# Kernel tuning notes

Measured on AMD Instinct MI355X. Metric: run time of the kernel, lower is better.

## Reference

```python
import jax, jax.numpy as jnp
import numpy as np

D = 64
N_NODES = 100000
N_EDGES = 1600000
N_GRAPHS = 64
IN_CH = 128
EDGE_DIM = 7
N_CONVS = 3  # layers after conv_first


def seg_softmax(logits, seg, n):
    m = jax.ops.segment_max(logits, seg, num_segments=n)
    e = jnp.exp(logits - m[seg])
    s = jax.ops.segment_sum(e, seg, num_segments=n)
    return e / (s[seg] + 1e-16)


def tconv(h, src, dst, edge_attr, Wq, bq, Wk, bk, Wv, bv, We, Ws, bs):
    # PyG TransformerConv, heads=1, concat=True, root_weight=True
    q = h @ Wq + bq          # [N, D]
    k = h @ Wk + bk
    v = h @ Wv + bv
    e = edge_attr @ We       # [E, D] (lin_edge has no bias)
    ke = k[src] + e          # key + edge per message
    alpha = jnp.sum(q[dst] * ke, axis=-1) / jnp.sqrt(jnp.float32(D))
    a = seg_softmax(alpha, dst, N_NODES)               # softmax over in-neighbors
    msg = a[:, None] * (v[src] + e)                    # [E, D]
    out = jax.ops.segment_sum(msg, dst, num_segments=N_NODES)
    return out + h @ Ws + bs                           # skip (lin_skip)


def setup_inputs() -> dict:
    key = jax.random.key(0)
    ks = iter(jax.random.split(key, 64))
    nrm = lambda shp, s=0.05: jax.random.normal(next(ks), shp, dtype=jnp.float32) * s
    inp = {}
    inp['x'] = jax.random.normal(next(ks), (N_NODES, IN_CH), dtype=jnp.float32)
    inp['edge_index'] = jax.random.randint(next(ks), (2, N_EDGES), 0, N_NODES, dtype=jnp.int32)
    inp['edge_attr'] = jax.random.normal(next(ks), (N_EDGES, EDGE_DIM), dtype=jnp.float32)
    inp['batch'] = jnp.sort(jax.random.randint(next(ks), (N_NODES,), 0, N_GRAPHS, dtype=jnp.int32))
    inp['y'] = jax.random.normal(next(ks), (N_GRAPHS, 6), dtype=jnp.float32)
    # conv_first (IN_CH -> D)
    inp['Wq0'] = nrm((IN_CH, D)); inp['bq0'] = jnp.zeros((D,), jnp.float32)
    inp['Wk0'] = nrm((IN_CH, D)); inp['bk0'] = jnp.zeros((D,), jnp.float32)
    inp['Wv0'] = nrm((IN_CH, D)); inp['bv0'] = jnp.zeros((D,), jnp.float32)
    inp['We0'] = nrm((EDGE_DIM, D))
    inp['Ws0'] = nrm((IN_CH, D)); inp['bs0'] = jnp.zeros((D,), jnp.float32)
    # stacked conv layers (D -> D), leading axis = layer
    inp['Wq'] = nrm((N_CONVS, D, D)); inp['bq'] = jnp.zeros((N_CONVS, D), jnp.float32)
    inp['Wk'] = nrm((N_CONVS, D, D)); inp['bk'] = jnp.zeros((N_CONVS, D), jnp.float32)
    inp['Wv'] = nrm((N_CONVS, D, D)); inp['bv'] = jnp.zeros((N_CONVS, D), jnp.float32)
    inp['We'] = nrm((N_CONVS, EDGE_DIM, D))
    inp['Ws'] = nrm((N_CONVS, D, D)); inp['bs'] = jnp.zeros((N_CONVS, D), jnp.float32)
    # gate_nn: Linear(D,D)+ReLU+Linear(D,1)
    inp['g1W'] = nrm((D, D)); inp['g1b'] = jnp.zeros((D,), jnp.float32)
    inp['g2W'] = nrm((D, 1)); inp['g2b'] = jnp.zeros((1,), jnp.float32)
    # 6 MLPs, each 64->32->16->8->1, stacked on leading expert axis
    inp['m0W'] = nrm((6, D, 32)); inp['m0b'] = jnp.zeros((6, 32), jnp.float32)
    inp['m1W'] = nrm((6, 32, 16)); inp['m1b'] = jnp.zeros((6, 16), jnp.float32)
    inp['m2W'] = nrm((6, 16, 8)); inp['m2b'] = jnp.zeros((6, 8), jnp.float32)
    inp['m3W'] = nrm((6, 8, 1)); inp['m3b'] = jnp.zeros((6, 1), jnp.float32)
    return inp


def reference(x, edge_attr, y, Wq0, bq0, Wk0, bk0, Wv0, bv0, We0, Ws0, bs0,
              Wq, bq, Wk, bk, Wv, bv, We, Ws, bs,
              g1W, g1b, g2W, g2b,
              m0W, m0b, m1W, m1b, m2W, m2b, m3W, m3b,
              edge_index, batch):
    src, dst = edge_index[0], edge_index[1]
    elu = jax.nn.elu
    outs = []
    h = elu(tconv(x, src, dst, edge_attr, Wq0, bq0, Wk0, bk0, Wv0, bv0, We0, Ws0, bs0))
    outs.append(h)
    for i in range(N_CONVS):
        h = tconv(h, src, dst, edge_attr, Wq[i], bq[i], Wk[i], bk[i],
                  Wv[i], bv[i], We[i], Ws[i], bs[i])
        if i != N_CONVS - 1:
            h = elu(h)
        outs.append(h)
    # JumpingKnowledge 'max'
    h = jnp.max(jnp.stack(outs, axis=0), axis=0)          # [N, D]
    # Global soft attention pooling
    gate = jax.nn.relu(h @ g1W + g1b) @ g2W + g2b         # [N, 1]
    gate = seg_softmax(gate[:, 0], batch, N_GRAPHS)[:, None]
    pooled = jax.ops.segment_sum(gate * h, batch, num_segments=N_GRAPHS)  # [G, D]
    # 6-way MLP ensemble (elu hidden)
    a = elu(jnp.einsum('gd,edh->egh', pooled, m0W) + m0b[:, None, :])
    a = elu(jnp.einsum('egh,ehk->egk', a, m1W) + m1b[:, None, :])
    a = elu(jnp.einsum('egk,ekj->egj', a, m2W) + m2b[:, None, :])
    preds = jnp.einsum('egj,ejo->ego', a, m3W) + m3b[:, None, :]  # [6, G, 1]
    preds = preds[:, :, 0].T                               # [G, 6]
    losses = jnp.sqrt(jnp.mean((preds - y) ** 2, axis=0))  # RMSE per target
    total_loss = jnp.sum(losses)
    return preds, total_loss
```

## Files before the change

### kernel.cpp

```cpp
#include <hip/hip_runtime.h>
#include <math.h>

#define N_NODES 100000
#define N_EDGES 1600000
#define N_GRAPHS 64
#define IN_CH 128
#define DIM 64
#define N_CONVS 3
#define NBLK 196
#define NPASS 8
#define PASS_SZ 12500

typedef const float* fp;
typedef unsigned int u32;
typedef unsigned short u16;
typedef __attribute__((ext_vector_type(8))) short short8v;
typedef __attribute__((ext_vector_type(4))) float f32x4;

__device__ inline u16 rne_bf16(float f) {
    u32 u = __float_as_uint(f);
    return (u16)((u + 0x7fffu + ((u >> 16) & 1u)) >> 16);
}
__device__ inline float bf16_f(u16 w) { return __uint_as_float((u32)w << 16); }
__device__ inline float bf16lo_f(u32 w) { return __uint_as_float(w << 16); }
__device__ inline float bf16hi_f(u32 w) { return __uint_as_float(w & 0xffff0000u); }
__device__ inline u32 f_enc(float f) {
    u32 u = __float_as_uint(f);
    return (u & 0x80000000u) ? ~u : (u | 0x80000000u);
}
__device__ inline float f_dec(u32 e) {
    u32 u = (e & 0x80000000u) ? (e & 0x7fffffffu) : ~e;
    return __uint_as_float(u);
}

__global__ __launch_bounds__(256) void count_kernel(const int* __restrict__ dst, int* __restrict__ cnt) {
    int j = blockIdx.x * 256 + threadIdx.x;
    if (j < N_EDGES) {
        int d = dst[j];
        if ((unsigned)d < N_NODES) atomicAdd(&cnt[d], 1);
    }
}

__global__ __launch_bounds__(512) void scan1_kernel(const int* __restrict__ cnt, int* __restrict__ rp,
                                                    int* __restrict__ blksum) {
    __shared__ int tmp[512];
    int t = threadIdx.x, i = blockIdx.x * 512 + t;
    int v0 = (i < N_NODES) ? cnt[i] : 0;
    tmp[t] = v0;
    __syncthreads();
    for (int off = 1; off < 512; off <<= 1) {
        int add = (t >= off) ? tmp[t - off] : 0;
        __syncthreads();
        tmp[t] += add;
        __syncthreads();
    }
    if (i < N_NODES) rp[i] = tmp[t] - v0;
    if (t == 511) blksum[blockIdx.x] = tmp[511];
}

__global__ __launch_bounds__(256) void scan2_kernel(int* __restrict__ blksum) {
    __shared__ int tmp[256];
    int t = threadIdx.x;
    int v0 = (t < NBLK) ? blksum[t] : 0;
    tmp[t] = v0;
    __syncthreads();
    for (int off = 1; off < 256; off <<= 1) {
        int add = (t >= off) ? tmp[t - off] : 0;
        __syncthreads();
        tmp[t] += add;
        __syncthreads();
    }
    if (t < NBLK) blksum[t] = tmp[t] - v0;
}

__global__ __launch_bounds__(512) void scan3_kernel(int* __restrict__ rp, const int* __restrict__ blksum,
                                                    int* __restrict__ cursor) {
    int t = threadIdx.x, i = blockIdx.x * 512 + t;
    if (i < N_NODES) {
        int v = rp[i] + blksum[blockIdx.x];
        rp[i] = v;
        cursor[i] = v;
    }
    if (i == 0) rp[N_NODES] = N_EDGES;
}

__global__ __launch_bounds__(256) void scatter_pass_kernel(const int* __restrict__ src,
                                                           const int* __restrict__ dst, fp ea,
                                                           int* __restrict__ cursor,
                                                           int* __restrict__ csr_src,
                                                           uint4* __restrict__ eab, int lo, int hi) {
    int j = blockIdx.x * 256 + threadIdx.x;
    if (j < N_EDGES) {
        int d = dst[j];
        if (d < lo || d >= hi || (unsigned)d >= N_NODES) return;
        int pos = atomicAdd(&cursor[d], 1);
        if ((unsigned)pos < N_EDGES) {
            int s = src[j];
            csr_src[pos] = ((unsigned)s < N_NODES) ? s : 0;
            size_t sb = (size_t)j * 7;
            u16 b[8];
#pragma unroll
            for (int c = 0; c < 7; ++c) b[c] = rne_bf16(ea[sb + c]);
            b[7] = 0;
            uint4 o;
            o.x = b[0] | ((u32)b[1] << 16);
            o.y = b[2] | ((u32)b[3] << 16);
            o.z = b[4] | ((u32)b[5] << 16);
            o.w = b[6] | ((u32)b[7] << 16);
            eab[pos] = o;
        }
    }
}

__global__ __launch_bounds__(256) void cvt_bf16_kernel(const float* __restrict__ in, u16* __restrict__ out,
                                                       int n4) {
    int i = blockIdx.x * 256 + threadIdx.x;
    if (i < n4) {
        float4 v = reinterpret_cast<const float4*>(in)[i];
        ushort4 o;
        o.x = rne_bf16(v.x); o.y = rne_bf16(v.y); o.z = rne_bf16(v.z); o.w = rne_bf16(v.w);
        reinterpret_cast<ushort4*>(out)[i] = o;
    }
}

__global__ __launch_bounds__(256) void packW_kernel(fp Wq, fp Wk, fp Wv, fp Ws, u16* __restrict__ Bp,
                                                    int K) {
    int total = (K / 32) * 16 * 512;
    int tid = blockIdx.x * 256 + threadIdx.x;
    if (tid >= total) return;
    int j = tid & 7, l = (tid >> 3) & 63, fragid = tid >> 9;
    int tk = fragid >> 4, gtn = fragid & 15;
    int k = tk * 32 + ((l >> 4) << 3) + j;
    int n = (gtn << 4) + (l & 15);
    int mat = n >> 6, cn = n & 63;
    fp W = mat == 0 ? Wq : mat == 1 ? Wk : mat == 2 ? Wv : Ws;
    Bp[tid] = rne_bf16(W[k * 64 + cn]);
}

template <int K>
__global__ __launch_bounds__(256) void gemm_mfma_kernel(
    const u16* __restrict__ A, const u16* __restrict__ Bp,
    fp bq, fp bk, fp bv, fp bs,
    u16* __restrict__ qb, u32* __restrict__ kvp, u16* __restrict__ skbb) {
    constexpr int NTK = K / 32;
    __shared__ u16 kls[32][64];
    int wave = threadIdx.x >> 6;
    int l = threadIdx.x & 63;
    int lr = l & 15, lg = l >> 4;
    int row0 = blockIdx.x * 32;
    short8v a[2][NTK];
#pragma unroll
    for (int mi = 0; mi < 2; ++mi)
#pragma unroll
        for (int tk = 0; tk < NTK; ++tk)
            a[mi][tk] = *reinterpret_cast<const short8v*>(
                &A[(size_t)(row0 + mi * 16 + lr) * K + tk * 32 + lg * 8]);
    f32x4 c[2][4] = {};
#pragma unroll
    for (int tn = 0; tn < 4; ++tn) {
        int gtn = wave * 4 + tn;
#pragma unroll
        for (int tk = 0; tk < NTK; ++tk) {
            short8v b = *reinterpret_cast<const short8v*>(&Bp[((size_t)(tk * 16 + gtn) * 64 + l) * 8]);
            c[0][tn] = __builtin_amdgcn_mfma_f32_16x16x32_bf16(a[0][tk], b, c[0][tn], 0, 0, 0);
            c[1][tn] = __builtin_amdgcn_mfma_f32_16x16x32_bf16(a[1][tk], b, c[1][tn], 0, 0, 0);
        }
    }
    fp bias = wave == 0 ? bq : wave == 1 ? bk : wave == 2 ? bv : bs;
    if (wave == 1) {
#pragma unroll
        for (int tn = 0; tn < 4; ++tn) {
            int cl = tn * 16 + lr;
            float bb = bias[cl];
#pragma unroll
            for (int mi = 0; mi < 2; ++mi)
#pragma unroll
                for (int r = 0; r < 4; ++r) {
                    int rr = mi * 16 + lg * 4 + r;
                    kls[rr][cl] = rne_bf16(c[mi][tn][r] + bb);
                }
        }
    }
    __syncthreads();
    if (wave == 1) return;
#pragma unroll
    for (int tn = 0; tn < 4; ++tn) {
        int cl = tn * 16 + lr;
        float bb = bias[cl];
#pragma unroll
        for (int mi = 0; mi < 2; ++mi)
#pragma unroll
            for (int r = 0; r < 4; ++r) {
                int rr = mi * 16 + lg * 4 + r;
                size_t row = row0 + rr;
                float val = c[mi][tn][r] + bb;
                if (wave == 0) qb[row * 64 + cl] = rne_bf16(val * 0.125f);
                else if (wave == 3) skbb[row * 64 + cl] = rne_bf16(val);
                else kvp[row * 64 + cl] = (u32)kls[rr][cl] | ((u32)rne_bf16(val) << 16);
            }
    }
}

__global__ __launch_bounds__(256) void node_kernel(
    const u16* __restrict__ qb, const u32* __restrict__ kvp,
    const u16* __restrict__ skbb, const uint4* __restrict__ eab, fp We,
    const int* __restrict__ row_ptr, const int* __restrict__ csr_src,
    u16* __restrict__ hb, u16* __restrict__ hmaxb, int act, int initmax) {
    int tid = threadIdx.x;
    int lane = tid & 63;
    int g = lane >> 4, fl = lane & 15;
    int n = blockIdx.x * 4 + (tid >> 6);
    int f0 = fl * 4;
    ushort4 qv = *reinterpret_cast<const ushort4*>(&qb[(size_t)n * 64 + f0]);
    float4 q4;
    q4.x = bf16_f(qv.x); q4.y = bf16_f(qv.y); q4.z = bf16_f(qv.z); q4.w = bf16_f(qv.w);
    float qw_own = 0.f;
#pragma unroll
    for (int c = 0; c < 7; ++c) {
        float4 w4 = *reinterpret_cast<const float4*>(&We[c * 64 + f0]);
        float t = q4.x * w4.x + q4.y * w4.y + q4.z * w4.z + q4.w * w4.w;
        t += __shfl_xor(t, 1);
        t += __shfl_xor(t, 2);
        t += __shfl_xor(t, 4);
        t += __shfl_xor(t, 8);
        if (fl == c) qw_own = t;
    }
    int beg = row_ptr[n], end = row_ptr[n + 1];
    float s = 0.f;
    float ax = 0.f, ay = 0.f, az = 0.f, aw = 0.f;
    float r_own = 0.f;

    for (int p0 = beg; p0 < end; p0 += 64) {
        int navail = end - p0;
        if (navail > 64) navail = 64;
        int sv = csr_src[p0 + (lane < navail ? lane : navail - 1)];
        for (int t = 0; t < navail; t += 4) {
            int eidx = t + g;
            bool valid = eidx < navail;
            int ec = valid ? eidx : navail - 1;
            int sn = __shfl(sv, ec);
            int pc = p0 + ec;
            uint4 kv4 = *reinterpret_cast<const uint4*>(&kvp[(size_t)sn * 64 + f0]);
            uint4 e4 = eab[pc];
            u32 w01 = (fl & 2) ? e4.y : e4.x;
            u32 w23 = (fl & 2) ? e4.w : e4.z;
            u32 wsel = (fl & 4) ? w23 : w01;
            float e_own = (fl & 1) ? bf16hi_f(wsel) : bf16lo_f(wsel);
            float kf0 = bf16lo_f(kv4.x), vf0 = bf16hi_f(kv4.x);
            float kf1 = bf16lo_f(kv4.y), vf1 = bf16hi_f(kv4.y);
            float kf2 = bf16lo_f(kv4.z), vf2 = bf16hi_f(kv4.z);
            float kf3 = bf16lo_f(kv4.w), vf3 = bf16hi_f(kv4.w);
            float d = q4.x * kf0 + q4.y * kf1 + q4.z * kf2 + q4.w * kf3 + qw_own * e_own;
            d += __shfl_xor(d, 1);
            d += __shfl_xor(d, 2);
            d += __shfl_xor(d, 4);
            d += __shfl_xor(d, 8);
            float pe = valid ? __expf(d) : 0.f;
            s += pe;
            ax += pe * vf0; ay += pe * vf1; az += pe * vf2; aw += pe * vf3;
            r_own += pe * e_own;
        }
    }
    s += __shfl_xor(s, 16); s += __shfl_xor(s, 32);
    ax += __shfl_xor(ax, 16); ax += __shfl_xor(ax, 32);
    ay += __shfl_xor(ay, 16); ay += __shfl_xor(ay, 32);
    az += __shfl_xor(az, 16); az += __shfl_xor(az, 32);
    aw += __shfl_xor(aw, 16); aw += __shfl_xor(aw, 32);
    r_own += __shfl_xor(r_own, 16); r_own += __shfl_xor(r_own, 32);

    float inv = 1.f / (s + 1e-16f);
    float o0 = ax, o1 = ay, o2 = az, o3 = aw;
#pragma unroll
    for (int c = 0; c < 7; ++c) {
        float rc = __shfl(r_own, c);
        o0 += We[c * 64 + f0 + 0] * rc;
        o1 += We[c * 64 + f0 + 1] * rc;
        o2 += We[c * 64 + f0 + 2] * rc;
        o3 += We[c * 64 + f0 + 3] * rc;
    }
    if (g != 0) return;
    ushort4 skv = *reinterpret_cast<const ushort4*>(&skbb[(size_t)n * 64 + f0]);
    float4 res;
    res.x = o0 * inv + bf16_f(skv.x);
    res.y = o1 * inv + bf16_f(skv.y);
    res.z = o2 * inv + bf16_f(skv.z);
    res.w = o3 * inv + bf16_f(skv.w);
    if (act) {
        res.x = res.x > 0.f ? res.x : (__expf(res.x) - 1.f);
        res.y = res.y > 0.f ? res.y : (__expf(res.y) - 1.f);
        res.z = res.z > 0.f ? res.z : (__expf(res.z) - 1.f);
        res.w = res.w > 0.f ? res.w : (__expf(res.w) - 1.f);
    }
    ushort4 hb4;
    hb4.x = rne_bf16(res.x); hb4.y = rne_bf16(res.y); hb4.z = rne_bf16(res.z); hb4.w = rne_bf16(res.w);
    *reinterpret_cast<ushort4*>(&hb[(size_t)n * 64 + f0]) = hb4;
    if (initmax) {
        *reinterpret_cast<ushort4*>(&hmaxb[(size_t)n * 64 + f0]) = hb4;
    } else {
        ushort4 hm4 = *reinterpret_cast<const ushort4*>(&hmaxb[(size_t)n * 64 + f0]);
        hm4.x = rne_bf16(fmaxf(bf16_f(hm4.x), res.x));
        hm4.y = rne_bf16(fmaxf(bf16_f(hm4.y), res.y));
        hm4.z = rne_bf16(fmaxf(bf16_f(hm4.z), res.z));
        hm4.w = rne_bf16(fmaxf(bf16_f(hm4.w), res.w));
        *reinterpret_cast<ushort4*>(&hmaxb[(size_t)n * 64 + f0]) = hm4;
    }
}

__global__ __launch_bounds__(256) void gate_kernel(const u16* __restrict__ h, fp g1W, fp g1b, fp g2W,
                                                   fp g2b, float* __restrict__ gate) {
    __shared__ float hs[4][64];
    int w = threadIdx.x >> 6, lane = threadIdx.x & 63;
    int n = blockIdx.x * 4 + w;
    hs[w][lane] = bf16_f(h[(size_t)n * 64 + lane]);
    __syncthreads();
    float a = 0.f;
    for (int f = 0; f < 64; ++f) a += hs[w][f] * g1W[f * 64 + lane];
    a = fmaxf(a + g1b[lane], 0.f);
    float val = a * g2W[lane];
#pragma unroll
    for (int off = 32; off; off >>= 1) val += __shfl_xor(val, off);
    if (lane == 0) gate[n] = val + g2b[0];
}

__global__ __launch_bounds__(256) void gmax_kernel(const float* __restrict__ gate,
                                                   const int* __restrict__ batch,
                                                   u32* __restrict__ gmaxEnc) {
    int i = blockIdx.x * 256 + threadIdx.x;
    if (i >= N_NODES) return;
    int lane = threadIdx.x & 63;
    int g = batch[i];
    u32 e = f_enc(gate[i]);
    int waveBase = i - lane;
    if (waveBase + 63 < N_NODES) {
        int g0 = __shfl(g, 0), g63 = __shfl(g, 63);
        if (g0 == g63) {
            u32 t = e;
#pragma unroll
            for (int off = 32; off; off >>= 1) t = max(t, (u32)__shfl_xor((int)t, off));
            if (lane == 0) atomicMax(&gmaxEnc[g], t);
            return;
        }
    }
    atomicMax(&gmaxEnc[g], e);
}

__global__ __launch_bounds__(256) void expsum_kernel(const int* __restrict__ batch,
                                                     const u32* __restrict__ gmaxEnc,
                                                     float* __restrict__ gate, float* __restrict__ gsum) {
    int i = blockIdx.x * 256 + threadIdx.x;
    if (i >= N_NODES) return;
    int lane = threadIdx.x & 63;
    int g = batch[i];
    float p = __expf(gate[i] - f_dec(gmaxEnc[g]));
    gate[i] = p;
    int waveBase = i - lane;
    bool fullWave = (waveBase + 63 < N_NODES);
    if (fullWave) {
        int g0 = __shfl(g, 0), g63 = __shfl(g, 63);
        if (g0 == g63) {
            float t = p;
#pragma unroll
            for (int off = 32; off; off >>= 1) t += __shfl_xor(t, off);
            if (lane == 0) atomicAdd(&gsum[g], t);
            return;
        }
    }
    atomicAdd(&gsum[g], p);
}

#define PCHUNK 256
__global__ __launch_bounds__(256) void pool_accum_kernel(const u16* __restrict__ h,
                                                         const float* __restrict__ gate,
                                                         const int* __restrict__ batch,
                                                         float* __restrict__ pooled) {
    int w = threadIdx.x >> 6, lane = threadIdx.x & 63;
    int base = blockIdx.x * PCHUNK;
    float acc = 0.f;
    int cur = -1;
    for (int t = 0; t < PCHUNK / 4; ++t) {
        int i = base + w + 4 * t;
        if (i >= N_NODES) break;
        int g = batch[i];
        if (g != cur) {
            if (cur >= 0) atomicAdd(&pooled[cur * 64 + lane], acc);
            acc = 0.f;
            cur = g;
        }
        acc += gate[i] * bf16_f(h[(size_t)i * 64 + lane]);
    }
    if (cur >= 0) atomicAdd(&pooled[cur * 64 + lane], acc);
}

__global__ __launch_bounds__(256) void mlp_kernel(const float* __restrict__ pooled,
                                                  const float* __restrict__ gsum, fp m0W, fp m0b, fp m1W,
                                                  fp m1b, fp m2W, fp m2b, fp m3W, fp m3b,
                                                  float* __restrict__ out) {
    int e = blockIdx.x, tid = threadIdx.x;
    __shared__ float P[64 * 64];
    __shared__ float A1[64 * 32];
    __shared__ float A2[64 * 16];
    __shared__ float A3[64 * 8];
    for (int i = tid; i < 64 * 64; i += 256) P[i] = pooled[i] / (gsum[i >> 6] + 1e-16f);
    __syncthreads();
    fp W0 = m0W + e * 64 * 32; fp B0 = m0b + e * 32;
    for (int i = tid; i < 64 * 32; i += 256) {
        int g = i >> 5, c = i & 31;
        float a = B0[c];
        for (int f = 0; f < 64; ++f) a += P[g * 64 + f] * W0[f * 32 + c];
        A1[i] = a > 0.f ? a : (__expf(a) - 1.f);
    }
    __syncthreads();
    fp W1 = m1W + e * 32 * 16; fp B1 = m1b + e * 16;
    for (int i = tid; i < 64 * 16; i += 256) {
        int g = i >> 4, c = i & 15;
        float a = B1[c];
        for (int f = 0; f < 32; ++f) a += A1[g * 32 + f] * W1[f * 16 + c];
        A2[i] = a > 0.f ? a : (__expf(a) - 1.f);
    }
    __syncthreads();
    fp W2 = m2W + e * 16 * 8; fp B2 = m2b + e * 8;
    for (int i = tid; i < 64 * 8; i += 256) {
        int g = i >> 3, c = i & 7;
        float a = B2[c];
        for (int f = 0; f < 16; ++f) a += A2[g * 16 + f] * W2[f * 8 + c];
        A3[i] = a > 0.f ? a : (__expf(a) - 1.f);
    }
    __syncthreads();
    fp W3 = m3W + e * 8;
    if (tid < 64) {
        int g = tid;
        float a = m3b[e];
        for (int j = 0; j < 8; ++j) a += A3[g * 8 + j] * W3[j];
        out[g * 6 + e] = a;
    }
}

__global__ __launch_bounds__(64) void loss_kernel(const float* __restrict__ preds, fp y,
                                                  float* __restrict__ out) {
    int lane = threadIdx.x;
    float lsum = 0.f;
    if (lane < 6) {
        float acc = 0.f;
        for (int g = 0; g < 64; ++g) {
            float d = preds[g * 6 + lane] - y[g * 6 + lane];
            acc += d * d;
        }
        lsum = sqrtf(acc / 64.f);
    }
#pragma unroll
    for (int off = 32; off; off >>= 1) lsum += __shfl_xor(lsum, off);
    if (lane == 0) out[384] = lsum;
}

extern "C" void kernel_launch(void* const* d_in, const int* in_sizes, int n_in, void* d_out, int out_size,
                              void* d_ws, size_t ws_size, hipStream_t stream) {
    bool dictOrder = (in_sizes[1] == 2 * N_EDGES);
    int iEI = dictOrder ? 1 : 33;
    int iEA = dictOrder ? 2 : 1;
    int iBT = dictOrder ? 3 : 34;
    int iY  = dictOrder ? 4 : 2;
    int w0  = dictOrder ? 5 : 3;

    fp x = (fp)d_in[0];
    const int* ei = (const int*)d_in[iEI];
    fp eattr = (fp)d_in[iEA];
    const int* batch = (const int*)d_in[iBT];
    fp y = (fp)d_in[iY];
    fp Wq0 = (fp)d_in[w0 + 0], bq0 = (fp)d_in[w0 + 1], Wk0 = (fp)d_in[w0 + 2], bk0 = (fp)d_in[w0 + 3];
    fp Wv0 = (fp)d_in[w0 + 4], bv0 = (fp)d_in[w0 + 5], We0 = (fp)d_in[w0 + 6];
    fp Ws0 = (fp)d_in[w0 + 7], bs0 = (fp)d_in[w0 + 8];
    fp Wq = (fp)d_in[w0 + 9], bq = (fp)d_in[w0 + 10], Wk = (fp)d_in[w0 + 11], bk = (fp)d_in[w0 + 12];
    fp Wv = (fp)d_in[w0 + 13], bv = (fp)d_in[w0 + 14], Wel = (fp)d_in[w0 + 15];
    fp Ws = (fp)d_in[w0 + 16], bs = (fp)d_in[w0 + 17];
    fp g1W = (fp)d_in[w0 + 18], g1b = (fp)d_in[w0 + 19], g2W = (fp)d_in[w0 + 20], g2b = (fp)d_in[w0 + 21];
    fp m0W = (fp)d_in[w0 + 22], m0b = (fp)d_in[w0 + 23], m1W = (fp)d_in[w0 + 24], m1b = (fp)d_in[w0 + 25];
    fp m2W = (fp)d_in[w0 + 26], m2b = (fp)d_in[w0 + 27], m3W = (fp)d_in[w0 + 28], m3b = (fp)d_in[w0 + 29];

    const int* srcArr = ei;
    const int* dstArr = ei + N_EDGES;

    char* wsp = (char*)d_ws;
    auto alloc = [&](size_t bytes) -> void* {
        void* p = (void*)wsp;
        wsp += (bytes + 255) & ~(size_t)255;
        return p;
    };
    u16* qb = (u16*)alloc((size_t)N_NODES * 64 * 2);
    u32* kvp = (u32*)alloc((size_t)N_NODES * 64 * 4);
    u16* skbb = (u16*)alloc((size_t)N_NODES * 64 * 2);
    u16* hb = (u16*)alloc((size_t)N_NODES * 64 * 2);
    u16* xb = (u16*)alloc((size_t)N_NODES * IN_CH * 2);
    u16* hmaxb = (u16*)alloc((size_t)N_NODES * 64 * 2);
    float* gate = (float*)alloc((size_t)N_NODES * 4);
    float* pooled = (float*)alloc(64 * 64 * 4);
    u32* gmaxEnc = (u32*)alloc(N_GRAPHS * 4);
    float* gsum = (float*)alloc(N_GRAPHS * 4);
    int* row_ptr = (int*)alloc((N_NODES + 1) * 4);
    int* cursor = (int*)alloc((size_t)N_NODES * 4);
    int* csr_src = (int*)alloc((size_t)N_EDGES * 4);
    uint4* eab = (uint4*)alloc((size_t)N_EDGES * 16);
    u16* Bp0 = (u16*)alloc((size_t)(IN_CH / 32) * 16 * 512 * 2);
    u16* Bp1 = (u16*)alloc((size_t)(DIM / 32) * 16 * 512 * 2);
    u16* Bp2 = (u16*)alloc((size_t)(DIM / 32) * 16 * 512 * 2);
    u16* Bp3 = (u16*)alloc((size_t)(DIM / 32) * 16 * 512 * 2);
    int* blksum = (int*)alloc(256 * 4);
    (void)ws_size;
    (void)n_in;

    float* outF = (float*)d_out;

    hipMemsetAsync(cursor, 0, (size_t)N_NODES * 4, stream);
    hipMemsetAsync(gmaxEnc, 0, N_GRAPHS * 4, stream);
    hipMemsetAsync(gsum, 0, N_GRAPHS * 4, stream);
    hipMemsetAsync(pooled, 0, 64 * 64 * 4, stream);
    count_kernel<<<(N_EDGES + 255) / 256, 256, 0, stream>>>(dstArr, cursor);
    scan1_kernel<<<NBLK, 512, 0, stream>>>(cursor, row_ptr, blksum);
    scan2_kernel<<<1, 256, 0, stream>>>(blksum);
    scan3_kernel<<<NBLK, 512, 0, stream>>>(row_ptr, blksum, cursor);
    for (int p = 0; p < NPASS; ++p)
        scatter_pass_kernel<<<(N_EDGES + 255) / 256, 256, 0, stream>>>(
            srcArr, dstArr, eattr, cursor, csr_src, eab, p * PASS_SZ, (p + 1) * PASS_SZ);
    cvt_bf16_kernel<<<(N_NODES * IN_CH / 4 + 255) / 256, 256, 0, stream>>>(x, xb, N_NODES * IN_CH / 4);
    packW_kernel<<<((IN_CH / 32) * 16 * 512 + 255) / 256, 256, 0, stream>>>(Wq0, Wk0, Wv0, Ws0, Bp0, IN_CH);
    u16* Bps[3] = {Bp1, Bp2, Bp3};
    for (int i = 0; i < N_CONVS; ++i)
        packW_kernel<<<((DIM / 32) * 16 * 512 + 255) / 256, 256, 0, stream>>>(
            Wq + i * 4096, Wk + i * 4096, Wv + i * 4096, Ws + i * 4096, Bps[i], DIM);

    int nodeGrid = N_NODES / 4;
    gemm_mfma_kernel<IN_CH><<<N_NODES / 32, 256, 0, stream>>>(xb, Bp0, bq0, bk0, bv0, bs0, qb, kvp, skbb);
    node_kernel<<<nodeGrid, 256, 0, stream>>>(qb, kvp, skbb, eab, We0, row_ptr, csr_src, hb, hmaxb, 1, 1);
    for (int i = 0; i < N_CONVS; ++i) {
        gemm_mfma_kernel<DIM><<<N_NODES / 32, 256, 0, stream>>>(hb, Bps[i], bq + i * 64, bk + i * 64,
                                                                bv + i * 64, bs + i * 64, qb, kvp, skbb);
        node_kernel<<<nodeGrid, 256, 0, stream>>>(qb, kvp, skbb, eab, Wel + i * 448, row_ptr,
                                                  csr_src, hb, hmaxb, (i < N_CONVS - 1) ? 1 : 0, 0);
    }
    gate_kernel<<<N_NODES / 4, 256, 0, stream>>>(hmaxb, g1W, g1b, g2W, g2b, gate);
    gmax_kernel<<<(N_NODES + 255) / 256, 256, 0, stream>>>(gate, batch, gmaxEnc);
    expsum_kernel<<<(N_NODES + 255) / 256, 256, 0, stream>>>(batch, gmaxEnc, gate, gsum);
    pool_accum_kernel<<<(N_NODES + PCHUNK - 1) / PCHUNK, 256, 0, stream>>>(hmaxb, gate, batch, pooled);
    mlp_kernel<<<6, 256, 0, stream>>>(pooled, gsum, m0W, m0b, m1W, m1b, m2W, m2b, m3W, m3b, outF);
    loss_kernel<<<1, 64, 0, stream>>>(outF, y, outF);
}
```

Baseline: 874.6 us.

## Map one node per 16-lane group instead of one node per wavefront

```diff
diff --git a/kernel.cpp b/kernel.cpp
--- a/kernel.cpp
+++ b/kernel.cpp
@@ -209,7 +209,8 @@
     int tid = threadIdx.x;
     int lane = tid & 63;
     int g = lane >> 4, fl = lane & 15;
-    int n = blockIdx.x * 4 + (tid >> 6);
+    int gbase = g << 4;
+    int n = blockIdx.x * 16 + (tid >> 6) * 4 + g;
     int f0 = fl * 4;
     ushort4 qv = *reinterpret_cast<const ushort4*>(&qb[(size_t)n * 64 + f0]);
     float4 q4;
@@ -230,16 +231,15 @@
     float ax = 0.f, ay = 0.f, az = 0.f, aw = 0.f;
     float r_own = 0.f;
 
-    for (int p0 = beg; p0 < end; p0 += 64) {
-        int navail = end - p0;
-        if (navail > 64) navail = 64;
-        int sv = csr_src[p0 + (lane < navail ? lane : navail - 1)];
-        for (int t = 0; t < navail; t += 4) {
-            int eidx = t + g;
-            bool valid = eidx < navail;
-            int ec = valid ? eidx : navail - 1;
-            int sn = __shfl(sv, ec);
-            int pc = p0 + ec;
+    for (int p = beg; p < end; p += 4) {
+        int svi = p + (fl & 3);
+        svi = svi < end ? svi : end - 1;
+        int sv = csr_src[svi];
+#pragma unroll
+        for (int j = 0; j < 4; ++j) {
+            int pj = p + j;
+            int pc = pj < end ? pj : end - 1;
+            int sn = __shfl(sv, gbase + j);
             uint4 kv4 = *reinterpret_cast<const uint4*>(&kvp[(size_t)sn * 64 + f0]);
             uint4 e4 = eab[pc];
             u32 w01 = (fl & 2) ? e4.y : e4.x;
@@ -255,30 +255,22 @@
             d += __shfl_xor(d, 2);
             d += __shfl_xor(d, 4);
             d += __shfl_xor(d, 8);
-            float pe = valid ? __expf(d) : 0.f;
+            float pe = (pj < end) ? __expf(d) : 0.f;
             s += pe;
             ax += pe * vf0; ay += pe * vf1; az += pe * vf2; aw += pe * vf3;
             r_own += pe * e_own;
         }
     }
-    s += __shfl_xor(s, 16); s += __shfl_xor(s, 32);
-    ax += __shfl_xor(ax, 16); ax += __shfl_xor(ax, 32);
-    ay += __shfl_xor(ay, 16); ay += __shfl_xor(ay, 32);
-    az += __shfl_xor(az, 16); az += __shfl_xor(az, 32);
-    aw += __shfl_xor(aw, 16); aw += __shfl_xor(aw, 32);
-    r_own += __shfl_xor(r_own, 16); r_own += __shfl_xor(r_own, 32);
-
     float inv = 1.f / (s + 1e-16f);
     float o0 = ax, o1 = ay, o2 = az, o3 = aw;
 #pragma unroll
     for (int c = 0; c < 7; ++c) {
-        float rc = __shfl(r_own, c);
+        float rc = __shfl(r_own, gbase + c);
         o0 += We[c * 64 + f0 + 0] * rc;
         o1 += We[c * 64 + f0 + 1] * rc;
         o2 += We[c * 64 + f0 + 2] * rc;
         o3 += We[c * 64 + f0 + 3] * rc;
     }
-    if (g != 0) return;
     ushort4 skv = *reinterpret_cast<const ushort4*>(&skbb[(size_t)n * 64 + f0]);
     float4 res;
     res.x = o0 * inv + bf16_f(skv.x);
@@ -527,7 +519,7 @@
         packW_kernel<<<((DIM / 32) * 16 * 512 + 255) / 256, 256, 0, stream>>>(
             Wq + i * 4096, Wk + i * 4096, Wv + i * 4096, Ws + i * 4096, Bps[i], DIM);
 
-    int nodeGrid = N_NODES / 4;
+    int nodeGrid = N_NODES / 16;
     gemm_mfma_kernel<IN_CH><<<N_NODES / 32, 256, 0, stream>>>(xb, Bp0, bq0, bk0, bv0, bs0, qb, kvp, skbb);
     node_kernel<<<nodeGrid, 256, 0, stream>>>(qb, kvp, skbb, eab, We0, row_ptr, csr_src, hb, hmaxb, 1, 1);
     for (int i = 0; i < N_CONVS; ++i) {
```

Measured after the change: 781.9 us. 10.6% less time.
